# Performance work log

Measured on AMD Instinct MI355X. Metric: run time of the kernel, lower is better.

Reference implementation:

```python
import jax, jax.numpy as jnp
import numpy as np

N_NODES, IN_DIM, HID, LAT, N_EDGES = 50000, 3000, 512, 30, 800000
NEG_SLOPE = 0.2


def setup_inputs() -> dict:
    key = jax.random.key(0)
    ks = jax.random.split(key, 6)
    x = jax.random.normal(ks[0], (N_NODES, IN_DIM), dtype=jnp.float32)
    edge_index = jax.random.randint(ks[1], (2, N_EDGES), 0, N_NODES, dtype=jnp.int64)
    # xavier-normal-ish scales
    W1 = jax.random.normal(ks[2], (IN_DIM, HID), dtype=jnp.float32) * 0.02
    W2 = jax.random.normal(ks[3], (HID, LAT), dtype=jnp.float32) * 0.06
    att_src = jax.random.normal(ks[4], (HID,), dtype=jnp.float32) * 0.1
    att_dst = jax.random.normal(ks[5], (HID,), dtype=jnp.float32) * 0.1
    return {"x": x, "edge_index": edge_index, "W1": W1, "W2": W2,
            "att_src": att_src, "att_dst": att_dst}


def _segment_softmax(e, seg, num_segments):
    # numerically stable softmax over variable-degree dst neighborhoods
    m = jax.ops.segment_max(e, seg, num_segments=num_segments)
    m = jnp.where(jnp.isfinite(m), m, 0.0)  # empty segments -> 0, harmless
    p = jnp.exp(e - m[seg])
    s = jax.ops.segment_sum(p, seg, num_segments=num_segments)
    return p / (s[seg] + 1e-16)


def reference(x, edge_index, W1, W2, att_src, att_dst):
    N = x.shape[0]
    src, dst = edge_index[0], edge_index[1]  # messages flow src(j) -> dst(i)

    # ---- conv1: full GAT layer (heads=1, no self-loops, no bias) ----
    h1 = x @ W1                                   # [N, 512]
    a_src = h1 @ att_src                          # [N]
    a_dst = h1 @ att_dst                          # [N]
    e = jax.nn.leaky_relu(a_src[src] + a_dst[dst], NEG_SLOPE)  # [E]
    alpha = _segment_softmax(e, dst, N)           # [E] (also tied attn for conv3)
    agg1 = jax.ops.segment_sum(h1[src] * alpha[:, None], dst, num_segments=N)
    x1 = jax.nn.elu(agg1)                         # [N, 512]

    # ---- conv2: attention=False -> plain linear projection ----
    x2 = x1 @ W2                                  # [N, 30] (latent embedding)

    # ---- conv3: tied weights (W2^T) + tied attention from conv1 ----
    h3 = x2 @ W2.T                                # [N, 512]
    agg3 = jax.ops.segment_sum(h3[src] * alpha[:, None], dst, num_segments=N)
    x3 = jax.nn.elu(agg3)

    # ---- conv4: attention=False, tied weights (W1^T) ----
    x4 = x3 @ W1.T                                # [N, in_channels]
    return (x2, x4)
```

## Files before the change

### kernel.cpp

```cpp
#include <hip/hip_runtime.h>

#define N_NODES 50000
#define IN_DIM  3000
#define HID     512
#define LAT     30
#define N_EDGES 800000
#define M_PAD   50048
#define K1_PAD  3008
#define N4_PAD  3072

typedef __bf16 bf16;
typedef unsigned int uint;
typedef __attribute__((ext_vector_type(4))) float f32x4;
typedef __attribute__((ext_vector_type(8))) bf16 bf16x8;

__device__ __forceinline__ float bf2f(bf16 b){ return (float)b; }

__device__ __forceinline__ void gl16(const void* g, void* l){
  __builtin_amdgcn_global_load_lds(
      (const __attribute__((address_space(1))) void*)g,
      (__attribute__((address_space(3))) void*)l, 16, 0, 0);
}

__device__ __forceinline__ int xcd_swz(int orig, int nwg){
  int q = nwg >> 3, r = nwg & 7;
  int xcd = orig & 7, lid = orig >> 3;
  return (xcd < r ? xcd*(q+1) : r*(q+1) + (xcd-r)*q) + lid;
}

__global__ void k_w1t(const float* __restrict__ W1, bf16* __restrict__ W1T){
  int k = blockIdx.x*256 + threadIdx.x;
  int n = blockIdx.y;
  if (k >= K1_PAD) return;
  float v = (k < IN_DIM) ? W1[(long)k*HID + n] : 0.f;
  W1T[(long)n*K1_PAD + k] = (bf16)v;
}
__global__ void k_w1p(const float* __restrict__ W1, bf16* __restrict__ W1P){
  int k = blockIdx.x*256 + threadIdx.x;
  int n = blockIdx.y;
  if (k >= HID) return;
  float v = (n < IN_DIM) ? W1[(long)n*HID + k] : 0.f;
  W1P[(long)n*HID + k] = (bf16)v;
}
__global__ void k_w2t(const float* __restrict__ W2, bf16* __restrict__ W2T){
  int k = blockIdx.x*256 + threadIdx.x;
  int n = blockIdx.y;
  if (k >= HID) return;
  float v = (n < LAT) ? W2[(long)k*LAT + n] : 0.f;
  W2T[(long)n*HID + k] = (bf16)v;
}
__global__ void k_w2p(const float* __restrict__ W2, bf16* __restrict__ W2P){
  int t = blockIdx.x*256 + threadIdx.x;
  if (t >= HID*32) return;
  int n = t >> 5, k = t & 31;
  W2P[t] = (bf16)((k < LAT) ? W2[(long)n*LAT + k] : 0.f);
}

__global__ __launch_bounds__(256) void k_cvt(const float* __restrict__ x, bf16* __restrict__ xb){
  int chunk = blockIdx.x*256 + threadIdx.x;
  int row = blockIdx.y;
  if (chunk >= K1_PAD/8) return;
  int c8 = chunk*8;
  bf16x8 o;
  if (row < N_NODES && c8 + 8 <= IN_DIM){
    float4 v0 = *(const float4*)(x + (long)row*IN_DIM + c8);
    float4 v1 = *(const float4*)(x + (long)row*IN_DIM + c8 + 4);
    o[0]=(bf16)v0.x; o[1]=(bf16)v0.y; o[2]=(bf16)v0.z; o[3]=(bf16)v0.w;
    o[4]=(bf16)v1.x; o[5]=(bf16)v1.y; o[6]=(bf16)v1.z; o[7]=(bf16)v1.w;
  } else {
    #pragma unroll
    for (int j=0;j<8;j++){
      int c = c8 + j;
      float v = (row < N_NODES && c < IN_DIM) ? x[(long)row*IN_DIM + c] : 0.f;
      o[j] = (bf16)v;
    }
  }
  *(bf16x8*)(xb + (long)row*K1_PAD + c8) = o;
}

template<bool C_F32, bool ELU>
__global__ __launch_bounds__(256) void gemm_glds(
    const bf16* __restrict__ A, const bf16* __restrict__ B, void* __restrict__ Cp,
    int lda, int ldb, int Ksteps, int Mvalid, int Nvalid, int ldc, int NBX)
{
  __shared__ bf16 Alds[2][128*32];
  __shared__ bf16 Blds[2][128*32];
  const int tid  = threadIdx.x;
  const int lane = tid & 63;
  const int w    = tid >> 6;
  const int wm   = (w >> 1) * 64, wn = (w & 1) * 64;
  const int wgid = xcd_swz(blockIdx.x, gridDim.x);
  const int col0 = (wgid % NBX) * 128, row0 = (wgid / NBX) * 128;

  f32x4 acc[4][4];
  #pragma unroll
  for (int mi=0;mi<4;mi++)
    #pragma unroll
    for (int ni=0;ni<4;ni++)
      acc[mi][ni] = (f32x4){0.f,0.f,0.f,0.f};

  const int sr = tid >> 2;
  const int sc = (tid & 3) * 16;
  const char* ga = (const char*)(A + (long)(row0 + sr) * lda) + sc;
  const char* gb = (const char*)(B + (long)(col0 + sr) * ldb) + sc;
  const long astep = (long)64 * lda * 2;
  const long bstep = (long)64 * ldb * 2;

#define STAGE_G(buf, ks) do{                                            \
    const long ko_ = (long)(ks) * 64;                                   \
    char* la_ = (char*)&Alds[buf][0] + sr*64 + sc;                      \
    char* lb_ = (char*)&Blds[buf][0] + sr*64 + sc;                      \
    gl16(ga + ko_,         la_);                                        \
    gl16(ga + ko_ + astep, la_ + 64*64);                                \
    gl16(gb + ko_,         lb_);                                        \
    gl16(gb + ko_ + bstep, lb_ + 64*64);                                \
  }while(0)

  STAGE_G(0, 0);

  for (int ks = 0; ks < Ksteps; ks++){
    const int cur = ks & 1;
    if (ks + 1 < Ksteps){
      STAGE_G(cur^1, ks+1);
      asm volatile("s_waitcnt vmcnt(4)" ::: "memory");
    } else {
      asm volatile("s_waitcnt vmcnt(0)" ::: "memory");
    }
    __builtin_amdgcn_s_barrier();

    const bf16* Ac = &Alds[cur][0];
    const bf16* Bc = &Blds[cur][0];
    bf16x8 af[4], bfr[4];
    #pragma unroll
    for (int mi=0;mi<4;mi++)
      af[mi] = *(const bf16x8*)&Ac[(wm + mi*16 + (lane & 15))*32 + (lane>>4)*8];
    #pragma unroll
    for (int ni=0;ni<4;ni++)
      bfr[ni] = *(const bf16x8*)&Bc[(wn + ni*16 + (lane & 15))*32 + (lane>>4)*8];
    #pragma unroll
    for (int mi=0;mi<4;mi++)
      #pragma unroll
      for (int ni=0;ni<4;ni++)
        acc[mi][ni] = __builtin_amdgcn_mfma_f32_16x16x32_bf16(af[mi], bfr[ni], acc[mi][ni], 0, 0, 0);

    __builtin_amdgcn_s_barrier();
  }
#undef STAGE_G

  const int crb  = (lane >> 4) * 4;
  const int ccol = lane & 15;
  #pragma unroll
  for (int mi=0;mi<4;mi++){
    #pragma unroll
    for (int v=0;v<4;v++){
      int r = row0 + wm + mi*16 + crb + v;
      if (r >= Mvalid) continue;
      #pragma unroll
      for (int ni=0;ni<4;ni++){
        int c = col0 + wn + ni*16 + ccol;
        if (c >= Nvalid) continue;
        float val = acc[mi][ni][v];
        if (ELU) val = (val > 0.f) ? val : expm1f(val);
        if (C_F32) ((float*)Cp)[(long)r*ldc + c] = val;
        else       ((bf16*)Cp)[(long)r*ldc + c] = (bf16)val;
      }
    }
  }
}

__global__ void k_attdots(const bf16* __restrict__ h1, const float* __restrict__ att_s,
                          const float* __restrict__ att_d, float* __restrict__ a_src,
                          float* __restrict__ a_dst){
  int gid = blockIdx.x * blockDim.x + threadIdx.x;
  int row = gid >> 6, lane = gid & 63;
  if (row >= N_NODES) return;
  bf16x8 hv = *(const bf16x8*)(h1 + (long)row*HID + lane*8);
  float s1 = 0.f, s2 = 0.f;
  #pragma unroll
  for (int j=0;j<8;j++){
    float h = bf2f(hv[j]);
    s1 = fmaf(h, att_s[lane*8+j], s1);
    s2 = fmaf(h, att_d[lane*8+j], s2);
  }
  #pragma unroll
  for (int o=32;o>0;o>>=1){ s1 += __shfl_down(s1,o); s2 += __shfl_down(s2,o); }
  if (lane == 0){ a_src[row] = s1; a_dst[row] = s2; }
}

__global__ void k_deg(const int* __restrict__ ei, int* __restrict__ deg){
  int e = blockIdx.x*256 + threadIdx.x;
  if (e >= N_EDGES) return;
  atomicAdd(&deg[ei[N_EDGES + e]], 1);
}

__global__ void k_scan(const int* __restrict__ deg, int* __restrict__ off, int* __restrict__ cur){
  const int n = M_PAD, T = 1024;
  int t = threadIdx.x;
  const int per = (n + T - 1) / T;
  int s0 = t*per, s1 = min(n, s0+per);
  int sum = 0;
  for (int i=s0;i<s1;i++) sum += deg[i];
  __shared__ int sd[1024];
  sd[t] = sum; __syncthreads();
  for (int o=1;o<T;o<<=1){
    int x = (t>=o) ? sd[t-o] : 0;
    __syncthreads();
    sd[t] += x;
    __syncthreads();
  }
  int run = sd[t] - sum;
  for (int i=s0;i<s1;i++){
    off[i] = run; cur[i] = run;
    run += deg[i];
  }
  if (s0 < n && s1 == n) off[n] = run;
}

__global__ void k_fill(const int* __restrict__ ei, int* __restrict__ cur,
                       int* __restrict__ csr_src, const float* __restrict__ a_s,
                       const float* __restrict__ a_d, float* __restrict__ p_e){
  int e = blockIdx.x*256 + threadIdx.x;
  if (e >= N_EDGES) return;
  int s = ei[e];
  int d = ei[N_EDGES + e];
  int pos = atomicAdd(&cur[d], 1);
  csr_src[pos] = s;
  float v = a_s[s] + a_d[d];
  v = (v > 0.f) ? v : 0.2f*v;
  p_e[pos] = __expf(v);
}

__global__ __launch_bounds__(512) void k_agg1(
    const int* __restrict__ off, const int* __restrict__ csr_src,
    const float* __restrict__ p_edge,
    const bf16* __restrict__ h1, bf16* __restrict__ x1,
    float* __restrict__ s_node)
{
  const int i = blockIdx.x;
  const int t = threadIdx.x;
  const int start = off[i];
  const int deg = off[i+1] - start;
  __shared__ float p_sh[512];
  __shared__ int   s_sh[512];

  float acc = 0.f, ssum = 0.f;
  for (int base=0; base<deg; base+=512){
    int cnt = min(512, deg-base);
    if (t < cnt){
      p_sh[t] = p_edge[start+base+t];
      s_sh[t] = csr_src[start+base+t];
    }
    __syncthreads();
    for (int k=0;k<cnt;k++){
      float pk = p_sh[k];
      ssum += pk;
      acc = fmaf(pk, bf2f(h1[(long)s_sh[k]*HID + t]), acc);
    }
    __syncthreads();
  }
  float val = acc / (ssum + 1e-16f);
  val = (val > 0.f) ? val : expm1f(val);
  x1[(long)i*HID + t] = (bf16)val;
  if (t == 0) s_node[i] = ssum;
}

__global__ void k_agg3(const int* __restrict__ off, const int* __restrict__ csr_src,
                       const float* __restrict__ p_edge, const float* __restrict__ s_node,
                       const float* __restrict__ x2, bf16* __restrict__ aggb)
{
  int i = blockIdx.x*8 + (threadIdx.x >> 5);
  int lane = threadIdx.x & 31;
  if (i >= M_PAD) return;
  float acc = 0.f;
  if (i < N_NODES){
    int s0 = off[i], d = off[i+1] - s0;
    for (int k=0;k<d;k++){
      int s = csr_src[s0+k];
      float pk = p_edge[s0+k];
      if (lane < LAT) acc = fmaf(pk, x2[(long)s*LAT + lane], acc);
    }
    acc *= 1.f/(s_node[i] + 1e-16f);
  }
  aggb[(long)i*32 + lane] = (bf16)((lane < LAT) ? acc : 0.f);
}

extern "C" void kernel_launch(void* const* d_in, const int* in_sizes, int n_in,
                              void* d_out, int out_size, void* d_ws, size_t ws_size,
                              hipStream_t stream)
{
  const float* x     = (const float*)d_in[0];
  const int*   ei    = (const int*)d_in[1];
  const float* W1    = (const float*)d_in[2];
  const float* W2    = (const float*)d_in[3];
  const float* att_s = (const float*)d_in[4];
  const float* att_d = (const float*)d_in[5];

  float* out_x2 = (float*)d_out;
  float* out_x4 = (float*)d_out + (long)N_NODES*LAT;

  bf16* xb = (bf16*)out_x4;
  bf16* h1 = xb + (long)M_PAD*K1_PAD;
  bf16* x1 = h1 + (long)M_PAD*HID;

  char* w = (char*)d_ws;
  bf16* W1T = (bf16*)w;  w += (long)HID*K1_PAD*2;
  bf16* W1P = (bf16*)w;  w += (long)N4_PAD*HID*2;
  bf16* W2T = (bf16*)w;  w += (long)128*HID*2;
  bf16* W2P = (bf16*)w;  w += (long)HID*32*2;
  bf16* x3  = (bf16*)w;  w += (long)M_PAD*HID*2;
  bf16* aggb= (bf16*)w;  w += (long)M_PAD*32*2;
  int* deg  = (int*)w;   w += (long)M_PAD*4;
  int* offs = (int*)w;   w += (long)(M_PAD+64)*4;
  int* cur  = (int*)w;   w += (long)M_PAD*4;
  int* csr  = (int*)w;   w += (long)N_EDGES*4;
  float* p_e = (float*)w; w += (long)N_EDGES*4;
  float* s_n = (float*)w; w += (long)M_PAD*4;
  float* a_s = (float*)w; w += (long)M_PAD*4;
  float* a_d = (float*)w; w += (long)M_PAD*4;

  k_w1t<<<dim3((K1_PAD+255)/256, HID), 256, 0, stream>>>(W1, W1T);
  k_w1p<<<dim3((HID+255)/256, N4_PAD), 256, 0, stream>>>(W1, W1P);
  k_w2t<<<dim3(2, 128), 256, 0, stream>>>(W2, W2T);
  k_w2p<<<(HID*32+255)/256, 256, 0, stream>>>(W2, W2P);
  k_cvt<<<dim3((K1_PAD/8+255)/256, M_PAD), 256, 0, stream>>>(x, xb);

  hipMemsetAsync(deg, 0, (size_t)M_PAD*4, stream);
  k_deg<<<(N_EDGES+255)/256, 256, 0, stream>>>(ei, deg);
  k_scan<<<1, 1024, 0, stream>>>(deg, offs, cur);

  gemm_glds<false,false><<<(HID/128)*(M_PAD/128), 256, 0, stream>>>(
      xb, W1T, h1, K1_PAD, K1_PAD, K1_PAD/32, N_NODES, HID, HID, HID/128);

  k_attdots<<<(N_NODES*64)/256, 256, 0, stream>>>(h1, att_s, att_d, a_s, a_d);

  k_fill<<<(N_EDGES+255)/256, 256, 0, stream>>>(ei, cur, csr, a_s, a_d, p_e);

  k_agg1<<<N_NODES, 512, 0, stream>>>(offs, csr, p_e, h1, x1, s_n);

  gemm_glds<true,false><<<1*(M_PAD/128), 256, 0, stream>>>(
      x1, W2T, out_x2, HID, HID, HID/32, N_NODES, LAT, LAT, 1);

  k_agg3<<<(M_PAD+7)/8, 256, 0, stream>>>(offs, csr, p_e, s_n, out_x2, aggb);
  gemm_glds<false,true><<<(HID/128)*(M_PAD/128), 256, 0, stream>>>(
      aggb, W2P, x3, 32, 32, 1, M_PAD, HID, HID, HID/128);

  gemm_glds<true,false><<<(N4_PAD/128)*(M_PAD/128), 256, 0, stream>>>(
      x3, W1P, out_x4, HID, HID, HID/32, N_NODES, IN_DIM, IN_DIM, N4_PAD/128);
}
```

Measured before the change: 1.211 ms.

## Add 256x128 eight-wave GEMM with swizzled LDS and wave-per-node aggregation

Adds a new 512-thread GEMM kernel with 256x128 tiles, BK=64, double-buffered global-to-LDS loads and an XOR-swizzled LDS layout. The W1 transposes are pre-swizzled to match, and the kernel is used for the two large GEMMs (x@W1 and x3@W1^T), with M padding raised to 50176. The conv1 aggregation now uses one 64-lane wave per node with 16-byte vector gathers instead of one 512-thread block per node. The goal is more data reuse and fewer LDS bank conflicts in the GEMMs, and better occupancy in the aggregation, at the cost of extra padding and more register pressure.

```diff
diff --git a/kernel.cpp b/kernel.cpp
--- a/kernel.cpp
+++ b/kernel.cpp
@@ -6,6 +6,7 @@
 #define LAT     30
 #define N_EDGES 800000
 #define M_PAD   50048
+#define M_PAD2  50176
 #define K1_PAD  3008
 #define N4_PAD  3072
 
@@ -33,14 +34,18 @@
   int n = blockIdx.y;
   if (k >= K1_PAD) return;
   float v = (k < IN_DIM) ? W1[(long)k*HID + n] : 0.f;
-  W1T[(long)n*K1_PAD + k] = (bf16)v;
+  int kt = k >> 6, c = (k >> 3) & 7, off = k & 7;
+  int p = c ^ (n & 7);
+  W1T[(long)n*K1_PAD + kt*64 + p*8 + off] = (bf16)v;
 }
 __global__ void k_w1p(const float* __restrict__ W1, bf16* __restrict__ W1P){
   int k = blockIdx.x*256 + threadIdx.x;
   int n = blockIdx.y;
   if (k >= HID) return;
   float v = (n < IN_DIM) ? W1[(long)n*HID + k] : 0.f;
-  W1P[(long)n*HID + k] = (bf16)v;
+  int kt = k >> 6, c = (k >> 3) & 7, off = k & 7;
+  int p = c ^ (n & 7);
+  W1P[(long)n*HID + kt*64 + p*8 + off] = (bf16)v;
 }
 __global__ void k_w2t(const float* __restrict__ W2, bf16* __restrict__ W2T){
   int k = blockIdx.x*256 + threadIdx.x;
@@ -76,6 +81,127 @@
     }
   }
   *(bf16x8*)(xb + (long)row*K1_PAD + c8) = o;
+}
+
+template<bool C_F32>
+__global__ __launch_bounds__(512) void gemm8(
+    const bf16* __restrict__ Agp, const bf16* __restrict__ Bgp, void* __restrict__ Cp,
+    int lda, int ldb, int NT, int Mvalid, int Nvalid, int ldc, int NBX)
+{
+  __shared__ bf16 Af[2][256*64];
+  __shared__ bf16 Bf[2][128*64];
+  const int tid  = threadIdx.x;
+  const int lane = tid & 63;
+  const int w    = tid >> 6;
+  const int wm   = (w >> 1) * 64;
+  const int wn   = (w & 1) * 64;
+  const int wgid = xcd_swz(blockIdx.x, gridDim.x);
+  const int col0 = (wgid % NBX) * 128, row0 = (wgid / NBX) * 256;
+
+  const int g   = lane >> 4;
+  const int rl  = lane & 15;
+  const int rx7 = rl & 7;
+
+  f32x4 acc[4][4];
+  #pragma unroll
+  for (int mi=0;mi<4;mi++)
+    #pragma unroll
+    for (int ni=0;ni<4;ni++)
+      acc[mi][ni] = (f32x4){0.f,0.f,0.f,0.f};
+
+  bf16x8 a[4][2], B0[4][2], B1[4][2];
+
+#define STAGE8(SLOT, T) do{                                                     \
+    const long kb_ = (long)(T)*64;                                              \
+    char* la_ = (char*)&Af[SLOT][0] + tid*16;                                   \
+    _Pragma("unroll")                                                           \
+    for (int i_=0;i_<4;i_++){                                                   \
+      int row_ = i_*64 + (tid>>3);                                              \
+      gl16(Agp + (long)(row0+row_)*lda + kb_ + (((tid&7)^(row_&7))<<3),         \
+           la_ + i_*8192);                                                      \
+    }                                                                           \
+    char* lb_ = (char*)&Bf[SLOT][0] + tid*16;                                   \
+    _Pragma("unroll")                                                           \
+    for (int i_=0;i_<2;i_++){                                                   \
+      int row_ = i_*64 + (tid>>3);                                              \
+      gl16(Bgp + (long)(col0+row_)*ldb + kb_ + ((tid&7)<<3),                    \
+           lb_ + i_*8192);                                                      \
+    }                                                                           \
+  }while(0)
+
+#define RD_A(S, Q, KS) (*(const bf16x8*)((const char*)&Af[S][0] + \
+    (wm + (Q)*16 + rl)*128 + ((((KS)*4 + g) ^ rx7)<<4)))
+#define RD_B(S, NQ, KS) (*(const bf16x8*)((const char*)&Bf[S][0] + \
+    (wn + (NQ)*16 + rl)*128 + ((((KS)*4 + g) ^ rx7)<<4)))
+
+#define PHASE8(Q, BC, BN, SLOTN, DORD) do{                                      \
+    __builtin_amdgcn_s_setprio(1);                                              \
+    _Pragma("unroll")                                                           \
+    for (int ni=0;ni<4;ni++)                                                    \
+      acc[Q][ni] = __builtin_amdgcn_mfma_f32_16x16x32_bf16(a[Q][0], BC[ni][0], acc[Q][ni],0,0,0); \
+    _Pragma("unroll")                                                           \
+    for (int ni=0;ni<4;ni++)                                                    \
+      acc[Q][ni] = __builtin_amdgcn_mfma_f32_16x16x32_bf16(a[Q][1], BC[ni][1], acc[Q][ni],0,0,0); \
+    __builtin_amdgcn_s_setprio(0);                                              \
+    if (DORD){                                                                  \
+      a[Q][0]  = RD_A(SLOTN, Q, 0);  a[Q][1]  = RD_A(SLOTN, Q, 1);              \
+      BN[Q][0] = RD_B(SLOTN, Q, 0);  BN[Q][1] = RD_B(SLOTN, Q, 1);              \
+    }                                                                           \
+  }while(0)
+
+#define ITER8(T, SLOT, SLOTN, BC, BN) do{                                       \
+    asm volatile("s_waitcnt vmcnt(0) lgkmcnt(0)" ::: "memory");                 \
+    __builtin_amdgcn_s_barrier();                                               \
+    __builtin_amdgcn_sched_barrier(0);                                          \
+    if ((T)+2 < NT) STAGE8(SLOT, (T)+2);                                        \
+    const bool dord_ = ((T)+1 < NT);                                            \
+    PHASE8(0, BC, BN, SLOTN, dord_);                                            \
+    PHASE8(1, BC, BN, SLOTN, dord_);                                            \
+    PHASE8(2, BC, BN, SLOTN, dord_);                                            \
+    PHASE8(3, BC, BN, SLOTN, dord_);                                            \
+  }while(0)
+
+  STAGE8(0, 0);
+  asm volatile("s_waitcnt vmcnt(0)" ::: "memory");
+  __builtin_amdgcn_s_barrier();
+  if (NT > 1) STAGE8(1, 1);
+  #pragma unroll
+  for (int q=0;q<4;q++){
+    a[q][0]  = RD_A(0, q, 0);  a[q][1]  = RD_A(0, q, 1);
+    B0[q][0] = RD_B(0, q, 0);  B0[q][1] = RD_B(0, q, 1);
+  }
+
+  int t = 0;
+  for (; t+1 < NT; t += 2){
+    ITER8(t,   0, 1, B0, B1);
+    ITER8(t+1, 1, 0, B1, B0);
+  }
+  if (t < NT) ITER8(t, 0, 1, B0, B1);
+
+#undef ITER8
+#undef PHASE8
+#undef RD_A
+#undef RD_B
+#undef STAGE8
+
+  const int crb  = (lane >> 4) * 4;
+  const int ccol = lane & 15;
+  #pragma unroll
+  for (int mi=0;mi<4;mi++){
+    #pragma unroll
+    for (int v=0;v<4;v++){
+      int r = row0 + wm + mi*16 + crb + v;
+      if (r >= Mvalid) continue;
+      #pragma unroll
+      for (int ni=0;ni<4;ni++){
+        int c = col0 + wn + ni*16 + ccol;
+        if (c >= Nvalid) continue;
+        float val = acc[mi][ni][v];
+        if (C_F32) ((float*)Cp)[(long)r*ldc + c] = val;
+        else       ((bf16*)Cp)[(long)r*ldc + c] = (bf16)val;
+      }
+    }
+  }
 }
 
 template<bool C_F32, bool ELU>
@@ -230,38 +356,41 @@
   p_e[pos] = __expf(v);
 }
 
-__global__ __launch_bounds__(512) void k_agg1(
+__global__ __launch_bounds__(256) void k_agg1w(
     const int* __restrict__ off, const int* __restrict__ csr_src,
     const float* __restrict__ p_edge,
     const bf16* __restrict__ h1, bf16* __restrict__ x1,
     float* __restrict__ s_node)
 {
-  const int i = blockIdx.x;
-  const int t = threadIdx.x;
+  const int i = blockIdx.x*4 + (threadIdx.x >> 6);
+  const int lane = threadIdx.x & 63;
+  if (i >= N_NODES) return;
   const int start = off[i];
   const int deg = off[i+1] - start;
-  __shared__ float p_sh[512];
-  __shared__ int   s_sh[512];
-
-  float acc = 0.f, ssum = 0.f;
-  for (int base=0; base<deg; base+=512){
-    int cnt = min(512, deg-base);
-    if (t < cnt){
-      p_sh[t] = p_edge[start+base+t];
-      s_sh[t] = csr_src[start+base+t];
-    }
-    __syncthreads();
-    for (int k=0;k<cnt;k++){
-      float pk = p_sh[k];
-      ssum += pk;
-      acc = fmaf(pk, bf2f(h1[(long)s_sh[k]*HID + t]), acc);
-    }
-    __syncthreads();
-  }
-  float val = acc / (ssum + 1e-16f);
-  val = (val > 0.f) ? val : expm1f(val);
-  x1[(long)i*HID + t] = (bf16)val;
-  if (t == 0) s_node[i] = ssum;
+
+  float acc[8];
+  #pragma unroll
+  for (int j=0;j<8;j++) acc[j] = 0.f;
+  float ssum = 0.f;
+
+  for (int k=0;k<deg;k++){
+    int s = csr_src[start+k];
+    float pk = p_edge[start+k];
+    ssum += pk;
+    bf16x8 hv = *(const bf16x8*)(h1 + (long)s*HID + lane*8);
+    #pragma unroll
+    for (int j=0;j<8;j++) acc[j] = fmaf(pk, bf2f(hv[j]), acc[j]);
+  }
+  float inv = 1.f/(ssum + 1e-16f);
+  bf16x8 o;
+  #pragma unroll
+  for (int j=0;j<8;j++){
+    float v = acc[j]*inv;
+    v = (v > 0.f) ? v : expm1f(v);
+    o[j] = (bf16)v;
+  }
+  *(bf16x8*)(x1 + (long)i*HID + lane*8) = o;
+  if (lane == 0) s_node[i] = ssum;
 }
 
 __global__ void k_agg3(const int* __restrict__ off, const int* __restrict__ csr_src,
@@ -270,7 +399,7 @@
 {
   int i = blockIdx.x*8 + (threadIdx.x >> 5);
   int lane = threadIdx.x & 31;
-  if (i >= M_PAD) return;
+  if (i >= M_PAD2) return;
   float acc = 0.f;
   if (i < N_NODES){
     int s0 = off[i], d = off[i+1] - s0;
@@ -299,7 +428,7 @@
   float* out_x4 = (float*)d_out + (long)N_NODES*LAT;
 
   bf16* xb = (bf16*)out_x4;
-  bf16* h1 = xb + (long)M_PAD*K1_PAD;
+  bf16* h1 = xb + (long)M_PAD2*K1_PAD;
   bf16* x1 = h1 + (long)M_PAD*HID;
 
   char* w = (char*)d_ws;
@@ -307,8 +436,8 @@
   bf16* W1P = (bf16*)w;  w += (long)N4_PAD*HID*2;
   bf16* W2T = (bf16*)w;  w += (long)128*HID*2;
   bf16* W2P = (bf16*)w;  w += (long)HID*32*2;
-  bf16* x3  = (bf16*)w;  w += (long)M_PAD*HID*2;
-  bf16* aggb= (bf16*)w;  w += (long)M_PAD*32*2;
+  bf16* x3  = (bf16*)w;  w += (long)M_PAD2*HID*2;
+  bf16* aggb= (bf16*)w;  w += (long)M_PAD2*32*2;
   int* deg  = (int*)w;   w += (long)M_PAD*4;
   int* offs = (int*)w;   w += (long)(M_PAD+64)*4;
   int* cur  = (int*)w;   w += (long)M_PAD*4;
@@ -322,28 +451,28 @@
   k_w1p<<<dim3((HID+255)/256, N4_PAD), 256, 0, stream>>>(W1, W1P);
   k_w2t<<<dim3(2, 128), 256, 0, stream>>>(W2, W2T);
   k_w2p<<<(HID*32+255)/256, 256, 0, stream>>>(W2, W2P);
-  k_cvt<<<dim3((K1_PAD/8+255)/256, M_PAD), 256, 0, stream>>>(x, xb);
+  k_cvt<<<dim3((K1_PAD/8+255)/256, M_PAD2), 256, 0, stream>>>(x, xb);
 
   hipMemsetAsync(deg, 0, (size_t)M_PAD*4, stream);
   k_deg<<<(N_EDGES+255)/256, 256, 0, stream>>>(ei, deg);
   k_scan<<<1, 1024, 0, stream>>>(deg, offs, cur);
 
-  gemm_glds<false,false><<<(HID/128)*(M_PAD/128), 256, 0, stream>>>(
-      xb, W1T, h1, K1_PAD, K1_PAD, K1_PAD/32, N_NODES, HID, HID, HID/128);
+  gemm8<false><<<(HID/128)*(M_PAD2/256), 512, 0, stream>>>(
+      xb, W1T, h1, K1_PAD, K1_PAD, K1_PAD/64, N_NODES, HID, HID, HID/128);
 
   k_attdots<<<(N_NODES*64)/256, 256, 0, stream>>>(h1, att_s, att_d, a_s, a_d);
 
   k_fill<<<(N_EDGES+255)/256, 256, 0, stream>>>(ei, cur, csr, a_s, a_d, p_e);
 
-  k_agg1<<<N_NODES, 512, 0, stream>>>(offs, csr, p_e, h1, x1, s_n);
+  k_agg1w<<<(N_NODES+3)/4, 256, 0, stream>>>(offs, csr, p_e, h1, x1, s_n);
 
   gemm_glds<true,false><<<1*(M_PAD/128), 256, 0, stream>>>(
       x1, W2T, out_x2, HID, HID, HID/32, N_NODES, LAT, LAT, 1);
 
-  k_agg3<<<(M_PAD+7)/8, 256, 0, stream>>>(offs, csr, p_e, s_n, out_x2, aggb);
-  gemm_glds<false,true><<<(HID/128)*(M_PAD/128), 256, 0, stream>>>(
-      aggb, W2P, x3, 32, 32, 1, M_PAD, HID, HID, HID/128);
-
-  gemm_glds<true,false><<<(N4_PAD/128)*(M_PAD/128), 256, 0, stream>>>(
-      x3, W1P, out_x4, HID, HID, HID/32, N_NODES, IN_DIM, IN_DIM, N4_PAD/128);
-}
+  k_agg3<<<(M_PAD2+7)/8, 256, 0, stream>>>(offs, csr, p_e, s_n, out_x2, aggb);
+  gemm_glds<false,true><<<(HID/128)*(M_PAD2/128), 256, 0, stream>>>(
+      aggb, W2P, x3, 32, 32, 1, M_PAD2, HID, HID, HID/128);
+
+  gemm8<true><<<(N4_PAD/128)*(M_PAD2/256), 512, 0, stream>>>(
+      x3, W1P, out_x4, HID, HID, HID/64, N_NODES, IN_DIM, IN_DIM, N4_PAD/128);
+}
```

Result: no change. 1.213 ms (+0.2%).
